# Kernel tuning notes

Measured on AMD Instinct MI355X. Metric: run time of the kernel, lower is better.

The kernel has to match this reference:

```python
import jax, jax.numpy as jnp
import numpy as np

N_NODES = 100000
N_EDGES = 3200000
IN_F, HID_F, OUT_F = 128, 128, 64
BN_EPS = 1e-5


def setup_inputs() -> dict:
    key = jax.random.key(0)
    ks = jax.random.split(key, 12)
    x = jax.random.normal(ks[0], (N_NODES, IN_F), dtype=jnp.float32)
    src = jax.random.randint(ks[1], (N_EDGES,), 0, N_NODES, dtype=jnp.int64)
    dst = jax.random.randint(ks[2], (N_EDGES,), 0, N_NODES, dtype=jnp.int64)
    s = 0.05
    W1 = jax.random.normal(ks[3], (IN_F, HID_F), dtype=jnp.float32) * s
    b1 = jnp.zeros((HID_F,), jnp.float32)
    W2 = jax.random.normal(ks[4], (HID_F, HID_F), dtype=jnp.float32) * s
    b2 = jnp.zeros((HID_F,), jnp.float32)
    W3 = jax.random.normal(ks[5], (HID_F, OUT_F), dtype=jnp.float32) * s
    b3 = jnp.zeros((OUT_F,), jnp.float32)
    gamma1 = jnp.ones((HID_F,), jnp.float32)
    beta1 = jnp.zeros((HID_F,), jnp.float32)
    gamma2 = jnp.ones((HID_F,), jnp.float32)
    beta2 = jnp.zeros((HID_F,), jnp.float32)
    return {"x": x, "src": src, "dst": dst,
            "W1": W1, "b1": b1, "W2": W2, "b2": b2, "W3": W3, "b3": b3,
            "gamma1": gamma1, "beta1": beta1, "gamma2": gamma2, "beta2": beta2}


def reference(x, src, dst, W1, b1, W2, b2, W3, b3, gamma1, beta1, gamma2, beta2):
    n = x.shape[0]
    ones = jnp.ones((src.shape[0],), x.dtype)
    # DGL GraphConv(norm='both'): symmetric normalization, degrees clamped to >=1
    deg_out = jax.ops.segment_sum(ones, src, num_segments=n)
    deg_in = jax.ops.segment_sum(ones, dst, num_segments=n)
    norm_s = jax.lax.rsqrt(jnp.maximum(deg_out, 1.0))[:, None]
    norm_d = jax.lax.rsqrt(jnp.maximum(deg_in, 1.0))[:, None]

    def conv(h, W, b):
        h = h * norm_s                                   # [N, F] scale by out-deg^{-1/2}
        m = jax.ops.segment_sum(h[src], dst, num_segments=n)  # SpMM aggregation
        return (m * norm_d) @ W + b

    def bn(h, g, b):  # BatchNorm1d, training-mode batch stats (biased var)
        mu = jnp.mean(h, axis=0)
        var = jnp.var(h, axis=0)
        return (h - mu) * jax.lax.rsqrt(var + BN_EPS) * g + b

    h = bn(jax.nn.relu(conv(x, W1, b1)), gamma1, beta1)
    h = bn(jax.nn.relu(conv(h, W2, b2)), gamma2, beta2)
    h = conv(h, W3, b3)
    return jax.nn.log_softmax(h, axis=1)
```

## Files before the change

### kernel.cpp

```cpp
#include <hip/hip_runtime.h>
#include <hip/hip_bf16.h>
#include <cstdint>

static constexpr int N = 100000;
static constexpr int E = 3200000;
static constexpr float BN_EPS = 1e-5f;
static constexpr int NBUCK = (N + 127) >> 7;
static constexpr int NBLK = 256;
static constexpr int CHUNK = E / NBLK;

static constexpr int NPW = 8;
static constexpr int NW2 = N / NPW;
static constexpr int AGG2_BLOCKS = NW2 / 4;
static constexpr int NSLICE = ((N - 1) >> 13) + 1;
static constexpr int NBKT = NSLICE * NPW;
static constexpr int BNRED_PER = (AGG2_BLOCKS + 63) / 64;

static constexpr size_t OFF_TOT_D = 0;
static constexpr size_t OFF_TOT_S = 3328;
static constexpr size_t OFF_DBASE = 6656;
static constexpr size_t OFF_SBASE = 9984;
static constexpr size_t OFF_CVEC  = 15360;
static constexpr size_t OFF_WT    = 16384;
static constexpr size_t OFF_PBASE = 49152;
static constexpr size_t OFF_PTOT  = 53248;
static constexpr size_t OFF_BNP2  = 82944;
static constexpr size_t OFF_EB    = 149504;
static constexpr size_t OFF_NORM_S= 2245632;
static constexpr size_t OFF_NORM_D= 2645632;
static constexpr size_t OFF_RP    = 3045632;
static constexpr size_t OFF_CNT_D = 3445760;
static constexpr size_t OFF_BNP   = OFF_CNT_D;
static constexpr size_t OFF_CNT_S = 4246528;
static constexpr size_t OFF_OFFD  = 5047296;
static constexpr size_t OFF_OFFS  = 5848064;
static constexpr size_t OFF_COL   = 6648832;
static constexpr size_t OFF_EPK   = 19448832;
static constexpr size_t OFF_SRCB  = 19448832;
static constexpr size_t OFF_PAIRS = 22648832;
static constexpr size_t OFF_H     = 35448832;
static constexpr size_t OFF_T     = 61048832;
static constexpr unsigned T_OFFU  = 61048832u;
static constexpr unsigned P_DUMMY  = 9437184u;
static constexpr unsigned C64      = 30524416u;
static constexpr size_t OFF_DUM128 = 9437184;
static constexpr size_t OFF_DUM64  = 35243008;

using short8  = __attribute__((ext_vector_type(8))) short;
using float4v = __attribute__((ext_vector_type(4))) float;

__device__ inline float bflo(unsigned v) { return __uint_as_float(v << 16); }
__device__ inline float bfhi(unsigned v) { return __uint_as_float(v & 0xffff0000u); }
__device__ inline unsigned short bfbits(float x) {
    __hip_bfloat16 h = __float2bfloat16(x);
    return *reinterpret_cast<unsigned short*>(&h);
}

__global__ __launch_bounds__(256) void k_count(const int* __restrict__ src,
                                               const int* __restrict__ dst,
                                               int* __restrict__ cnt_s,
                                               int* __restrict__ cnt_d) {
    __shared__ int hs[NBUCK], hd[NBUCK];
    int tid = threadIdx.x, blk = blockIdx.x;
    for (int b = tid; b < NBUCK; b += 256) { hs[b] = 0; hd[b] = 0; }
    __syncthreads();
    int e0 = blk * CHUNK, e1 = min(E, e0 + CHUNK);
    for (int e = e0 + tid; e < e1; e += 256) {
        atomicAdd(&hs[src[e] >> 7], 1);
        atomicAdd(&hd[dst[e] >> 7], 1);
    }
    __syncthreads();
    for (int b = tid; b < NBUCK; b += 256) {
        cnt_s[blk * NBUCK + b] = hs[b];
        cnt_d[blk * NBUCK + b] = hd[b];
    }
}

__global__ __launch_bounds__(256) void k_scanA2(const int* __restrict__ cnt_d,
                                                const int* __restrict__ cnt_s,
                                                int* __restrict__ offd,
                                                int* __restrict__ offs,
                                                int* __restrict__ tot_d,
                                                int* __restrict__ tot_s) {
    __shared__ int sd[256];
    int which = (blockIdx.x >= NBUCK) ? 1 : 0;
    int b = blockIdx.x - which * NBUCK;
    const int* cnt = which ? cnt_s : cnt_d;
    int* off = which ? offs : offd;
    int* tot = which ? tot_s : tot_d;
    int tid = threadIdx.x;
    int v = cnt[tid * NBUCK + b];
    sd[tid] = v;
    __syncthreads();
    for (int o = 1; o < 256; o <<= 1) {
        int t = (tid >= o) ? sd[tid - o] : 0;
        __syncthreads();
        sd[tid] += t;
        __syncthreads();
    }
    off[tid * NBUCK + b] = sd[tid] - v;
    if (tid == 255) tot[b] = sd[255];
}

__global__ __launch_bounds__(1024) void k_scanB(const int* __restrict__ tot_d,
                                                const int* __restrict__ tot_s,
                                                int* __restrict__ dbase,
                                                int* __restrict__ sbase) {
    __shared__ int sd[1024], ss[1024];
    int tid = threadIdx.x;
    int vd = (tid < NBUCK) ? tot_d[tid] : 0;
    int vs = (tid < NBUCK) ? tot_s[tid] : 0;
    sd[tid] = vd; ss[tid] = vs;
    __syncthreads();
    for (int o = 1; o < 1024; o <<= 1) {
        int td = (tid >= o) ? sd[tid - o] : 0;
        int ts = (tid >= o) ? ss[tid - o] : 0;
        __syncthreads();
        sd[tid] += td; ss[tid] += ts;
        __syncthreads();
    }
    if (tid < NBUCK) { dbase[tid] = sd[tid] - vd; sbase[tid] = ss[tid] - vs; }
    if (tid == 0) { dbase[NBUCK] = E; sbase[NBUCK] = E; }
}

__global__ __launch_bounds__(256) void k_scatter(const int* __restrict__ src,
                                                 const int* __restrict__ dst,
                                                 const int* __restrict__ dbase,
                                                 const int* __restrict__ sbase,
                                                 const int* __restrict__ offd,
                                                 const int* __restrict__ offs,
                                                 unsigned* __restrict__ pairs,
                                                 unsigned char* __restrict__ srcb) {
    __shared__ int cd[NBUCK], cs[NBUCK];
    int tid = threadIdx.x, blk = blockIdx.x;
    for (int b = tid; b < NBUCK; b += 256) {
        cd[b] = dbase[b] + offd[blk * NBUCK + b];
        cs[b] = sbase[b] + offs[blk * NBUCK + b];
    }
    __syncthreads();
    int e0 = blk * CHUNK, e1 = min(E, e0 + CHUNK);
    for (int e = e0 + tid; e < e1; e += 256) {
        int s = src[e], d = dst[e];
        int pd = atomicAdd(&cd[d >> 7], 1);
        pairs[pd] = (unsigned)s | ((unsigned)(d & 127) << 20);
        int ps = atomicAdd(&cs[s >> 7], 1);
        srcb[ps] = (unsigned char)(s & 127);
    }
}

__global__ __launch_bounds__(256) void k_build(const unsigned* __restrict__ pairs,
                                               const unsigned char* __restrict__ srcb,
                                               const int* __restrict__ dbase,
                                               const int* __restrict__ sbase,
                                               int* __restrict__ rp,
                                               float* __restrict__ norm_d,
                                               float* __restrict__ norm_s,
                                               int* __restrict__ col,
                                               int* __restrict__ eb,
                                               int* __restrict__ ptot) {
    __shared__ int cnt[128], scn[128], lcur[128];
    __shared__ int wpe[16], wps[16];
    int b = blockIdx.x, tid = threadIdx.x, node0 = b << 7;
    int nmax = min(128, N - node0);
    if (tid < 128) cnt[tid] = 0;
    __syncthreads();
    int sb = sbase[b], se = sbase[b + 1];
    for (int e = sb + tid; e < se; e += 256) atomicAdd(&cnt[srcb[e]], 1);
    __syncthreads();
    if (tid < nmax) norm_s[node0 + tid] = rsqrtf(fmaxf((float)cnt[tid], 1.0f));
    __syncthreads();
    if (tid < 128) cnt[tid] = 0;
    __syncthreads();
    int beg = dbase[b], end = dbase[b + 1];
    for (int e = beg + tid; e < end; e += 256) atomicAdd(&cnt[pairs[e] >> 20], 1);
    __syncthreads();
    if (tid < 128) scn[tid] = cnt[tid];
    if (tid < 16) {
        int s = 0;
#pragma unroll
        for (int i = 0; i < 8; ++i) s += cnt[tid * 8 + i];
        wpe[tid] = (s + 7) & ~7;
    }
    __syncthreads();
    for (int o = 1; o < 128; o <<= 1) {
        int t = (tid < 128 && tid >= o) ? scn[tid - o] : 0;
        __syncthreads();
        if (tid < 128) scn[tid] += t;
        __syncthreads();
    }
    if (tid == 0) {
        int run = 0;
#pragma unroll
        for (int k = 0; k < 16; ++k) { int c = wpe[k]; wps[k] = run; run += c; }
        ptot[b] = run;
    }
    __syncthreads();
    if (tid < 16) eb[b * 16 + tid] = wps[tid];
    if (tid < nmax) {
        int excl = beg + scn[tid] - cnt[tid];
        rp[node0 + tid] = excl;
        lcur[tid] = excl;
        norm_d[node0 + tid] = rsqrtf(fmaxf((float)cnt[tid], 1.0f));
    }
    if (b == 0 && tid == 0) rp[N] = E;
    __syncthreads();
    for (int e = beg + tid; e < end; e += 256) {
        unsigned p = pairs[e];
        int pos = atomicAdd(&lcur[p >> 20], 1);
        col[pos] = (int)(p & 0xFFFFFu);
    }
}

__global__ __launch_bounds__(1024) void k_scanP(const int* __restrict__ ptot,
                                                int* __restrict__ pbase,
                                                int* __restrict__ eb) {
    __shared__ int sd[1024];
    int tid = threadIdx.x;
    int v = (tid < NBUCK) ? ptot[tid] : 0;
    sd[tid] = v;
    __syncthreads();
    for (int o = 1; o < 1024; o <<= 1) {
        int t = (tid >= o) ? sd[tid - o] : 0;
        __syncthreads();
        sd[tid] += t;
        __syncthreads();
    }
    if (tid < NBUCK) pbase[tid] = sd[tid] - v;
    if (tid == 1023) { pbase[NBUCK] = sd[1023]; eb[NW2] = sd[1023]; }
}

__global__ __launch_bounds__(256) void k_eprep(const int* __restrict__ col,
                                               const int* __restrict__ rp,
                                               const int* __restrict__ pbase,
                                               int* __restrict__ eb,
                                               unsigned* __restrict__ epk) {
    __shared__ int cnt[4][NBKT];
    int tid = threadIdx.x, wave = tid >> 6, lane = tid & 63;
    int w = blockIdx.x * 4 + wave;
    int n0 = w * NPW;
    for (int k = lane; k < NBKT; k += 64) cnt[wave][k] = 0;
    int rpl[NPW + 1];
#pragma unroll
    for (int j = 0; j <= NPW; ++j) rpl[j] = rp[n0 + j];
#pragma unroll
    for (int j = 0; j < NPW; ++j)
        for (int e = rpl[j] + lane; e < rpl[j + 1]; e += 64)
            atomicAdd(&cnt[wave][(((unsigned)col[e]) >> 13) * NPW + j], 1);
    if (lane == 0) {
        int base = pbase[n0 >> 7] + eb[w];
        eb[w] = base;
        int run = base;
        for (int k = 0; k < NBKT; ++k) { int c = cnt[wave][k]; cnt[wave][k] = run; run += c; }
        int padend = base + ((rpl[NPW] - rpl[0] + 7) & ~7);
        for (int q = run; q < padend; ++q) epk[q] = P_DUMMY;
    }
#pragma unroll
    for (int j = 0; j < NPW; ++j)
        for (int e = rpl[j] + lane; e < rpl[j + 1]; e += 64) {
            unsigned c = (unsigned)col[e];
            int pos = atomicAdd(&cnt[wave][(c >> 13) * NPW + j], 1);
            epk[pos] = T_OFFU + (c << 8) + (unsigned)j;
        }
}

template <bool AFFINE>
__global__ __launch_bounds__(64) void k_wprep(const float* __restrict__ W,
                                              const float* __restrict__ part2,
                                              const float* __restrict__ gamma,
                                              const float* __restrict__ beta,
                                              int fout,
                                              unsigned short* __restrict__ Wt,
                                              float* __restrict__ cvec,
                                              unsigned* __restrict__ dz256,
                                              unsigned* __restrict__ dz64) {
    int n = blockIdx.x, k = threadIdx.x;
    if (!AFFINE && n == 0) {
        dz256[k] = 0u;
        if (k < 32) dz64[k] = 0u;
    }
    float a0 = 1.f, c0 = 0.f, a1 = 1.f, c1 = 0.f;
    if (AFFINE) {
        int l0 = ((k & 1) ? 128 : 0) + (k >> 1);
        int m0 = ((k & 1) ? 192 : 64) + (k >> 1);
        int l1 = l0 + 32, m1 = m0 + 32;
        float s0 = 0.f, q0 = 0.f, s1 = 0.f, q1 = 0.f;
        for (int b = 0; b < 64; ++b) {
            const float* r = part2 + b * 256;
            s0 += r[l0]; q0 += r[m0];
            s1 += r[l1]; q1 += r[m1];
        }
        float mu0 = s0 * (1.0f / N), var0 = q0 * (1.0f / N) - mu0 * mu0;
        a0 = gamma[k] * rsqrtf(var0 + BN_EPS);
        c0 = beta[k] - mu0 * a0;
        float mu1 = s1 * (1.0f / N), var1 = q1 * (1.0f / N) - mu1 * mu1;
        a1 = gamma[k + 64] * rsqrtf(var1 + BN_EPS);
        c1 = beta[k + 64] - mu1 * a1;
    }
    float w0 = W[k * fout + n], w1 = W[(k + 64) * fout + n];
    Wt[n * 128 + k] = bfbits(a0 * w0);
    Wt[n * 128 + k + 64] = bfbits(a1 * w1);
    float cv = c0 * w0 + c1 * w1;
    for (int o = 32; o; o >>= 1) cv += __shfl_xor(cv, o);
    if (k == 0) cvec[n] = cv;
}

template <typename TIn, int FOUT>
__global__ __launch_bounds__(256) void k_gemm(const TIn* __restrict__ in,
                                              const unsigned short* __restrict__ Wt,
                                              const float* __restrict__ cvec,
                                              const float* __restrict__ ns,
                                              unsigned short* __restrict__ out) {
    constexpr int PK = 72;
    __shared__ __align__(16) unsigned short Xs[128 * PK];
    __shared__ __align__(16) unsigned short Wsh[FOUT * PK];
    const int tid = threadIdx.x;
    const int r0 = blockIdx.x * 128;
    const int wave = tid >> 6, lane = tid & 63;
    const int l16 = lane & 15, quad = lane >> 4;
    constexpr int MT = (FOUT == 128) ? 4 : 2;
    constexpr int NT = 4;
    const int wm = (FOUT == 128) ? (wave >> 1) : wave;
    const int wn = (FOUT == 128) ? (wave & 1) : 0;
    const int mbase = wm * (MT * 16);
    const int nbase = wn * 64;

    float4v acc[MT][NT];
#pragma unroll
    for (int mt = 0; mt < MT; ++mt)
#pragma unroll
        for (int nt = 0; nt < NT; ++nt) acc[mt][nt] = (float4v){0.f, 0.f, 0.f, 0.f};

    for (int kb = 0; kb < 128; kb += 64) {
        __syncthreads();
        for (int i = tid; i < 128 * 8; i += 256) {
            int row = i >> 3, j = i & 7;
            int grow = r0 + row;
            if constexpr (sizeof(TIn) == 4) {
                short8 p = {0, 0, 0, 0, 0, 0, 0, 0};
                if (grow < N) {
                    const float* g = (const float*)in + (size_t)grow * 128 + kb + j * 8;
                    float4 f0 = *(const float4*)g;
                    float4 f1 = *(const float4*)(g + 4);
                    p[0] = (short)bfbits(f0.x); p[1] = (short)bfbits(f0.y);
                    p[2] = (short)bfbits(f0.z); p[3] = (short)bfbits(f0.w);
                    p[4] = (short)bfbits(f1.x); p[5] = (short)bfbits(f1.y);
                    p[6] = (short)bfbits(f1.z); p[7] = (short)bfbits(f1.w);
                }
                *(short8*)&Xs[row * PK + j * 8] = p;
            } else {
                uint4 v = make_uint4(0, 0, 0, 0);
                if (grow < N)
                    v = *(const uint4*)((const unsigned short*)in + (size_t)grow * 128 + kb + j * 8);
                *(uint4*)&Xs[row * PK + j * 8] = v;
            }
        }
        for (int i = tid; i < FOUT * 8; i += 256) {
            int n = i >> 3, j = i & 7;
            uint4 v = *(const uint4*)&Wt[n * 128 + kb + j * 8];
            *(uint4*)&Wsh[n * PK + j * 8] = v;
        }
        __syncthreads();
#pragma unroll
        for (int ks = 0; ks < 64; ks += 32) {
            short8 af[MT], bfr[NT];
#pragma unroll
            for (int mt = 0; mt < MT; ++mt)
                af[mt] = *(const short8*)&Xs[(mbase + mt * 16 + l16) * PK + ks + quad * 8];
#pragma unroll
            for (int nt = 0; nt < NT; ++nt)
                bfr[nt] = *(const short8*)&Wsh[(nbase + nt * 16 + l16) * PK + ks + quad * 8];
#pragma unroll
            for (int mt = 0; mt < MT; ++mt)
#pragma unroll
                for (int nt = 0; nt < NT; ++nt)
                    acc[mt][nt] = __builtin_amdgcn_mfma_f32_16x16x32_bf16(
                        af[mt], bfr[nt], acc[mt][nt], 0, 0, 0);
        }
    }
    float cv[NT];
#pragma unroll
    for (int nt = 0; nt < NT; ++nt) cv[nt] = cvec[nbase + nt * 16 + l16];
#pragma unroll
    for (int mt = 0; mt < MT; ++mt) {
#pragma unroll
        for (int r = 0; r < 4; ++r) {
            int row = r0 + mbase + mt * 16 + quad * 4 + r;
            if (row < N) {
                float s = ns[row];
#pragma unroll
                for (int nt = 0; nt < NT; ++nt)
                    out[(size_t)row * FOUT + nbase + nt * 16 + l16] =
                        bfbits((acc[mt][nt][r] + cv[nt]) * s);
            }
        }
    }
}

__global__ __launch_bounds__(256, 8) void k_agg128s(const char* wsb,
                                                    const int* __restrict__ eb,
                                                    const unsigned* __restrict__ epk,
                                                    const float* __restrict__ norm_d,
                                                    const float* __restrict__ bias,
                                                    unsigned* Hu,
                                                    float* __restrict__ part) {
    __shared__ float acc[4][NPW][128];
    const int tid = threadIdx.x, wave = tid >> 6, lane = tid & 63;
    const int w = blockIdx.x * 4 + wave;
    const int n0 = w * NPW;
    float2* a2 = reinterpret_cast<float2*>(&acc[wave][0][0]) + lane;
#pragma unroll
    for (int j = 0; j < NPW; ++j) a2[j * 64] = make_float2(0.f, 0.f);
    const unsigned lane4 = (unsigned)(lane << 2);
    int e = __builtin_amdgcn_readfirstlane(eb[w]);
    const int e1 = __builtin_amdgcn_readfirstlane(eb[w + 1]);
    int cur = 0;
    float a0 = 0.f, a1 = 0.f;
    for (; e < e1; e += 8) {
        unsigned p[8];
#pragma unroll
        for (int i = 0; i < 8; ++i) p[i] = epk[e + i];
        int dl[8];
#pragma unroll
        for (int i = 0; i < 8; ++i) dl[i] = __builtin_amdgcn_readfirstlane((int)(p[i] & 7u));
        float f0[8], f1[8];
#pragma unroll
        for (int i = 0; i < 8; ++i) {
            unsigned v = *(const unsigned*)(wsb + (p[i] & 0xFFFFFF00u) + lane4);
            f0[i] = bflo(v); f1[i] = bfhi(v);
        }
#pragma unroll
        for (int i = 0; i < 8; ++i) asm volatile("" :: "v"(f0[i]), "v"(f1[i]));
        __builtin_amdgcn_sched_barrier(0);
#pragma unroll
        for (int i = 0; i < 8; ++i) {
            if (dl[i] != cur) {
                float2 t = a2[cur * 64];
                t.x += a0; t.y += a1;
                a2[cur * 64] = t;
                cur = dl[i]; a0 = 0.f; a1 = 0.f;
            }
            a0 += f0[i]; a1 += f1[i];
        }
    }
    {
        float2 t = a2[cur * 64];
        t.x += a0; t.y += a1;
        a2[cur * 64] = t;
    }
    float s0 = 0.f, q0 = 0.f, s1 = 0.f, q1 = 0.f;
    const float bb0 = bias[2 * lane], bb1 = bias[2 * lane + 1];
#pragma unroll
    for (int j = 0; j < NPW; ++j) {
        int n = n0 + j;
        float2 a = a2[j * 64];
        float nd = norm_d[n];
        float r0 = fmaxf(a.x * nd + bb0, 0.0f);
        float r1 = fmaxf(a.y * nd + bb1, 0.0f);
        Hu[(size_t)n * 64 + lane] = ((unsigned)bfbits(r1) << 16) | bfbits(r0);
        s0 += r0; q0 += r0 * r0; s1 += r1; q1 += r1 * r1;
    }
    __syncthreads();
    float* red = &acc[0][0][0];
    red[wave * 256 + lane] = s0;
    red[wave * 256 + 64 + lane] = q0;
    red[wave * 256 + 128 + lane] = s1;
    red[wave * 256 + 192 + lane] = q1;
    __syncthreads();
    float t = red[tid] + red[256 + tid] + red[512 + tid] + red[768 + tid];
    part[blockIdx.x * 256 + tid] = t;
}

__global__ __launch_bounds__(256) void k_bnred(const float* __restrict__ part,
                                               float* __restrict__ part2) {
    int b = blockIdx.x, tid = threadIdx.x;
    float s = 0.f;
    for (int i = 0; i < BNRED_PER; ++i) {
        int r = b * BNRED_PER + i;
        if (r < AGG2_BLOCKS) s += part[r * 256 + tid];
    }
    part2[b * 256 + tid] = s;
}

__global__ __launch_bounds__(256, 8) void k_agg64s(const char* wsb,
                                                   const int* __restrict__ eb,
                                                   const unsigned* __restrict__ epk,
                                                   const float* __restrict__ norm_d,
                                                   const float* __restrict__ b3,
                                                   float* __restrict__ out) {
    __shared__ float acc[4][NPW][64];
    const int tid = threadIdx.x, wave = tid >> 6, lane = tid & 63;
    const int w = blockIdx.x * 4 + wave;
    const int n0 = w * NPW;
    float* a1p = &acc[wave][0][0] + lane;
#pragma unroll
    for (int j = 0; j < NPW; ++j) a1p[j * 64] = 0.f;
    const unsigned lane2 = (unsigned)(lane << 1);
    int e = __builtin_amdgcn_readfirstlane(eb[w]);
    const int e1 = __builtin_amdgcn_readfirstlane(eb[w + 1]);
    int cur = 0;
    float a0 = 0.f;
    for (; e < e1; e += 8) {
        unsigned p[8];
#pragma unroll
        for (int i = 0; i < 8; ++i) p[i] = epk[e + i];
        int dl[8];
#pragma unroll
        for (int i = 0; i < 8; ++i) dl[i] = __builtin_amdgcn_readfirstlane((int)(p[i] & 7u));
        float f[8];
#pragma unroll
        for (int i = 0; i < 8; ++i) {
            unsigned u = *(const unsigned short*)(wsb + (((p[i] >> 1) & 0xFFFFFF80u) + C64) + lane2);
            f[i] = __uint_as_float(u << 16);
        }
#pragma unroll
        for (int i = 0; i < 8; ++i) asm volatile("" :: "v"(f[i]));
        __builtin_amdgcn_sched_barrier(0);
#pragma unroll
        for (int i = 0; i < 8; ++i) {
            if (dl[i] != cur) {
                a1p[cur * 64] += a0;
                cur = dl[i]; a0 = 0.f;
            }
            a0 += f[i];
        }
    }
    a1p[cur * 64] += a0;
    const float bb = b3[lane];
#pragma unroll
    for (int j = 0; j < NPW; ++j) {
        int n = n0 + j;
        float z = a1p[j * 64] * norm_d[n] + bb;
        float m = z;
        for (int o = 32; o; o >>= 1) m = fmaxf(m, __shfl_xor(m, o));
        float ex = __expf(z - m);
        float ssum = ex;
        for (int o = 32; o; o >>= 1) ssum += __shfl_xor(ssum, o);
        out[(size_t)n * 64 + lane] = z - m - __logf(ssum);
    }
}

extern "C" void kernel_launch(void* const* d_in, const int* in_sizes, int n_in,
                              void* d_out, int out_size, void* d_ws, size_t ws_size,
                              hipStream_t stream) {
    const float* x  = (const float*)d_in[0];
    const int* src  = (const int*)d_in[1];
    const int* dst  = (const int*)d_in[2];
    const float* W1 = (const float*)d_in[3];
    const float* b1 = (const float*)d_in[4];
    const float* W2 = (const float*)d_in[5];
    const float* b2 = (const float*)d_in[6];
    const float* W3 = (const float*)d_in[7];
    const float* b3 = (const float*)d_in[8];
    const float* g1 = (const float*)d_in[9];
    const float* be1= (const float*)d_in[10];
    const float* g2 = (const float*)d_in[11];
    const float* be2= (const float*)d_in[12];
    float* out = (float*)d_out;

    char* ws = (char*)d_ws;
    int* tot_d = (int*)(ws + OFF_TOT_D);
    int* tot_s = (int*)(ws + OFF_TOT_S);
    int* dbase = (int*)(ws + OFF_DBASE);
    int* sbase = (int*)(ws + OFF_SBASE);
    float* cvec = (float*)(ws + OFF_CVEC);
    unsigned short* Wt = (unsigned short*)(ws + OFF_WT);
    int* pbase = (int*)(ws + OFF_PBASE);
    int* ptot  = (int*)(ws + OFF_PTOT);
    float* bnp2 = (float*)(ws + OFF_BNP2);
    int* eb = (int*)(ws + OFF_EB);
    float* bnp = (float*)(ws + OFF_BNP);
    float* norm_s = (float*)(ws + OFF_NORM_S);
    float* norm_d = (float*)(ws + OFF_NORM_D);
    int* rp = (int*)(ws + OFF_RP);
    int* cnt_d = (int*)(ws + OFF_CNT_D);
    int* cnt_s = (int*)(ws + OFF_CNT_S);
    int* offd = (int*)(ws + OFF_OFFD);
    int* offs = (int*)(ws + OFF_OFFS);
    int* col = (int*)(ws + OFF_COL);
    unsigned char* srcb = (unsigned char*)(ws + OFF_SRCB);
    unsigned* pairs = (unsigned*)(ws + OFF_PAIRS);
    unsigned* epk = (unsigned*)(ws + OFF_EPK);
    unsigned* dz256 = (unsigned*)(ws + OFF_DUM128);
    unsigned* dz64  = (unsigned*)(ws + OFF_DUM64);
    unsigned short* H = (unsigned short*)(ws + OFF_H);
    unsigned short* T = (unsigned short*)(ws + OFF_T);

    k_count<<<NBLK, 256, 0, stream>>>(src, dst, cnt_s, cnt_d);
    k_scanA2<<<2 * NBUCK, 256, 0, stream>>>(cnt_d, cnt_s, offd, offs, tot_d, tot_s);
    k_scanB<<<1, 1024, 0, stream>>>(tot_d, tot_s, dbase, sbase);
    k_scatter<<<NBLK, 256, 0, stream>>>(src, dst, dbase, sbase, offd, offs, pairs, srcb);
    k_build<<<NBUCK, 256, 0, stream>>>(pairs, srcb, dbase, sbase, rp, norm_d, norm_s, col, eb, ptot);
    k_scanP<<<1, 1024, 0, stream>>>(ptot, pbase, eb);
    k_eprep<<<AGG2_BLOCKS, 256, 0, stream>>>(col, rp, pbase, eb, epk);

    const int gemm_grid = (N + 127) / 128;

    k_wprep<false><<<128, 64, 0, stream>>>(W1, nullptr, nullptr, nullptr, 128, Wt, cvec, dz256, dz64);
    k_gemm<float, 128><<<gemm_grid, 256, 0, stream>>>(x, Wt, cvec, norm_s, T);
    k_agg128s<<<AGG2_BLOCKS, 256, 0, stream>>>(ws, eb, epk, norm_d, b1, (unsigned*)H, bnp);
    k_bnred<<<64, 256, 0, stream>>>(bnp, bnp2);

    k_wprep<true><<<128, 64, 0, stream>>>(W2, bnp2, g1, be1, 128, Wt, cvec, nullptr, nullptr);
    k_gemm<__hip_bfloat16, 128><<<gemm_grid, 256, 0, stream>>>((const __hip_bfloat16*)H, Wt, cvec, norm_s, T);
    k_agg128s<<<AGG2_BLOCKS, 256, 0, stream>>>(ws, eb, epk, norm_d, b2, (unsigned*)H, bnp);
    k_bnred<<<64, 256, 0, stream>>>(bnp, bnp2);

    k_wprep<true><<<64, 64, 0, stream>>>(W3, bnp2, g2, be2, 64, Wt, cvec, nullptr, nullptr);
    k_gemm<__hip_bfloat16, 64><<<gemm_grid, 256, 0, stream>>>((const __hip_bfloat16*)H, Wt, cvec, norm_s, T);
    k_agg64s<<<AGG2_BLOCKS, 256, 0, stream>>>(ws, eb, epk, norm_d, b3, out);
}
```

Measured before the change: 607.3 us.

## Software-pipeline edge gathers in aggregation kernels with double-buffered batches

The aggregation loops in the 128-wide and 64-wide SpMM kernels now keep two batches of 8 edges in flight: the next batch's indices and feature rows are loaded while the previous batch is accumulated, with sched_barriers enforcing the ordering. To give the loop whole 16-edge iterations, per-wave edge segment padding is raised from multiples of 8 to multiples of 16, in both the prefix-sum sizing and the dummy-fill code. The aim is to hide gather latency at the cost of more registers per wave, which can lower occupancy, and extra padded dummy edges to process.

```diff
diff --git a/kernel.cpp b/kernel.cpp
--- a/kernel.cpp
+++ b/kernel.cpp
@@ -179,7 +179,7 @@
         int s = 0;
 #pragma unroll
         for (int i = 0; i < 8; ++i) s += cnt[tid * 8 + i];
-        wpe[tid] = (s + 7) & ~7;
+        wpe[tid] = (s + 15) & ~15;
     }
     __syncthreads();
     for (int o = 1; o < 128; o <<= 1) {
@@ -251,7 +251,7 @@
         eb[w] = base;
         int run = base;
         for (int k = 0; k < NBKT; ++k) { int c = cnt[wave][k]; cnt[wave][k] = run; run += c; }
-        int padend = base + ((rpl[NPW] - rpl[0] + 7) & ~7);
+        int padend = base + ((rpl[NPW] - rpl[0] + 15) & ~15);
         for (int q = run; q < padend; ++q) epk[q] = P_DUMMY;
     }
 #pragma unroll
@@ -415,37 +415,67 @@
     const int e1 = __builtin_amdgcn_readfirstlane(eb[w + 1]);
     int cur = 0;
     float a0 = 0.f, a1 = 0.f;
-    for (; e < e1; e += 8) {
-        unsigned p[8];
-#pragma unroll
-        for (int i = 0; i < 8; ++i) p[i] = epk[e + i];
-        int dl[8];
-#pragma unroll
-        for (int i = 0; i < 8; ++i) dl[i] = __builtin_amdgcn_readfirstlane((int)(p[i] & 7u));
-        float f0[8], f1[8];
+    if (e < e1) {
+        unsigned pa[8], pb[8];
+        int da[8], db[8];
+        float fa0[8], fa1[8], fb0[8], fb1[8];
+#pragma unroll
+        for (int i = 0; i < 8; ++i) pa[i] = epk[e + i];
+#pragma unroll
+        for (int i = 0; i < 8; ++i) da[i] = __builtin_amdgcn_readfirstlane((int)(pa[i] & 7u));
 #pragma unroll
         for (int i = 0; i < 8; ++i) {
-            unsigned v = *(const unsigned*)(wsb + (p[i] & 0xFFFFFF00u) + lane4);
-            f0[i] = bflo(v); f1[i] = bfhi(v);
-        }
-#pragma unroll
-        for (int i = 0; i < 8; ++i) asm volatile("" :: "v"(f0[i]), "v"(f1[i]));
-        __builtin_amdgcn_sched_barrier(0);
-#pragma unroll
-        for (int i = 0; i < 8; ++i) {
-            if (dl[i] != cur) {
-                float2 t = a2[cur * 64];
-                t.x += a0; t.y += a1;
-                a2[cur * 64] = t;
-                cur = dl[i]; a0 = 0.f; a1 = 0.f;
-            }
-            a0 += f0[i]; a1 += f1[i];
-        }
-    }
-    {
-        float2 t = a2[cur * 64];
-        t.x += a0; t.y += a1;
-        a2[cur * 64] = t;
+            unsigned v = *(const unsigned*)(wsb + (pa[i] & 0xFFFFFF00u) + lane4);
+            fa0[i] = bflo(v); fa1[i] = bfhi(v);
+        }
+        for (; e + 16 <= e1; e += 16) {
+#pragma unroll
+            for (int i = 0; i < 8; ++i) pb[i] = epk[e + 8 + i];
+#pragma unroll
+            for (int i = 0; i < 8; ++i) db[i] = __builtin_amdgcn_readfirstlane((int)(pb[i] & 7u));
+#pragma unroll
+            for (int i = 0; i < 8; ++i) {
+                unsigned v = *(const unsigned*)(wsb + (pb[i] & 0xFFFFFF00u) + lane4);
+                fb0[i] = bflo(v); fb1[i] = bfhi(v);
+            }
+#pragma unroll
+            for (int i = 0; i < 8; ++i) asm volatile("" :: "v"(fa0[i]), "v"(fa1[i]));
+            __builtin_amdgcn_sched_barrier(0);
+#pragma unroll
+            for (int i = 0; i < 8; ++i) {
+                if (da[i] != cur) {
+                    float2 t = a2[cur * 64]; t.x += a0; t.y += a1; a2[cur * 64] = t;
+                    cur = da[i]; a0 = 0.f; a1 = 0.f;
+                }
+                a0 += fa0[i]; a1 += fa1[i];
+            }
+            __builtin_amdgcn_sched_barrier(0);
+            {
+                int en = (e + 16 < e1) ? (e + 16) : (e1 - 8);
+#pragma unroll
+                for (int i = 0; i < 8; ++i) pa[i] = epk[en + i];
+#pragma unroll
+                for (int i = 0; i < 8; ++i) da[i] = __builtin_amdgcn_readfirstlane((int)(pa[i] & 7u));
+#pragma unroll
+                for (int i = 0; i < 8; ++i) {
+                    unsigned v = *(const unsigned*)(wsb + (pa[i] & 0xFFFFFF00u) + lane4);
+                    fa0[i] = bflo(v); fa1[i] = bfhi(v);
+                }
+            }
+#pragma unroll
+            for (int i = 0; i < 8; ++i) asm volatile("" :: "v"(fb0[i]), "v"(fb1[i]));
+            __builtin_amdgcn_sched_barrier(0);
+#pragma unroll
+            for (int i = 0; i < 8; ++i) {
+                if (db[i] != cur) {
+                    float2 t = a2[cur * 64]; t.x += a0; t.y += a1; a2[cur * 64] = t;
+                    cur = db[i]; a0 = 0.f; a1 = 0.f;
+                }
+                a0 += fb0[i]; a1 += fb1[i];
+            }
+            __builtin_amdgcn_sched_barrier(0);
+        }
+        float2 t = a2[cur * 64]; t.x += a0; t.y += a1; a2[cur * 64] = t;
     }
     float s0 = 0.f, q0 = 0.f, s1 = 0.f, q1 = 0.f;
     const float bb0 = bias[2 * lane], bb1 = bias[2 * lane + 1];
@@ -499,32 +529,62 @@
     const int e1 = __builtin_amdgcn_readfirstlane(eb[w + 1]);
     int cur = 0;
     float a0 = 0.f;
-    for (; e < e1; e += 8) {
-        unsigned p[8];
-#pragma unroll
-        for (int i = 0; i < 8; ++i) p[i] = epk[e + i];
-        int dl[8];
-#pragma unroll
-        for (int i = 0; i < 8; ++i) dl[i] = __builtin_amdgcn_readfirstlane((int)(p[i] & 7u));
-        float f[8];
+    if (e < e1) {
+        unsigned pa[8], pb[8];
+        int da[8], db[8];
+        float fa[8], fb[8];
+#pragma unroll
+        for (int i = 0; i < 8; ++i) pa[i] = epk[e + i];
+#pragma unroll
+        for (int i = 0; i < 8; ++i) da[i] = __builtin_amdgcn_readfirstlane((int)(pa[i] & 7u));
 #pragma unroll
         for (int i = 0; i < 8; ++i) {
-            unsigned u = *(const unsigned short*)(wsb + (((p[i] >> 1) & 0xFFFFFF80u) + C64) + lane2);
-            f[i] = __uint_as_float(u << 16);
-        }
-#pragma unroll
-        for (int i = 0; i < 8; ++i) asm volatile("" :: "v"(f[i]));
-        __builtin_amdgcn_sched_barrier(0);
-#pragma unroll
-        for (int i = 0; i < 8; ++i) {
-            if (dl[i] != cur) {
-                a1p[cur * 64] += a0;
-                cur = dl[i]; a0 = 0.f;
-            }
-            a0 += f[i];
-        }
-    }
-    a1p[cur * 64] += a0;
+            unsigned u = *(const unsigned short*)(wsb + (((pa[i] >> 1) & 0xFFFFFF80u) + C64) + lane2);
+            fa[i] = __uint_as_float(u << 16);
+        }
+        for (; e + 16 <= e1; e += 16) {
+#pragma unroll
+            for (int i = 0; i < 8; ++i) pb[i] = epk[e + 8 + i];
+#pragma unroll
+            for (int i = 0; i < 8; ++i) db[i] = __builtin_amdgcn_readfirstlane((int)(pb[i] & 7u));
+#pragma unroll
+            for (int i = 0; i < 8; ++i) {
+                unsigned u = *(const unsigned short*)(wsb + (((pb[i] >> 1) & 0xFFFFFF80u) + C64) + lane2);
+                fb[i] = __uint_as_float(u << 16);
+            }
+#pragma unroll
+            for (int i = 0; i < 8; ++i) asm volatile("" :: "v"(fa[i]));
+            __builtin_amdgcn_sched_barrier(0);
+#pragma unroll
+            for (int i = 0; i < 8; ++i) {
+                if (da[i] != cur) { a1p[cur * 64] += a0; cur = da[i]; a0 = 0.f; }
+                a0 += fa[i];
+            }
+            __builtin_amdgcn_sched_barrier(0);
+            {
+                int en = (e + 16 < e1) ? (e + 16) : (e1 - 8);
+#pragma unroll
+                for (int i = 0; i < 8; ++i) pa[i] = epk[en + i];
+#pragma unroll
+                for (int i = 0; i < 8; ++i) da[i] = __builtin_amdgcn_readfirstlane((int)(pa[i] & 7u));
+#pragma unroll
+                for (int i = 0; i < 8; ++i) {
+                    unsigned u = *(const unsigned short*)(wsb + (((pa[i] >> 1) & 0xFFFFFF80u) + C64) + lane2);
+                    fa[i] = __uint_as_float(u << 16);
+                }
+            }
+#pragma unroll
+            for (int i = 0; i < 8; ++i) asm volatile("" :: "v"(fb[i]));
+            __builtin_amdgcn_sched_barrier(0);
+#pragma unroll
+            for (int i = 0; i < 8; ++i) {
+                if (db[i] != cur) { a1p[cur * 64] += a0; cur = db[i]; a0 = 0.f; }
+                a0 += fb[i];
+            }
+            __builtin_amdgcn_sched_barrier(0);
+        }
+        a1p[cur * 64] += a0;
+    }
     const float bb = b3[lane];
 #pragma unroll
     for (int j = 0; j < NPW; ++j) {
```

Result: no change. 596.0 us (median of 2 runs) (-1.9%).
